# Optimization experiments

Measured on AMD Instinct MI355X. Metric: run time of the kernel, lower is better.

## Reference

```python
import jax, jax.numpy as jnp
import numpy as np

B, LQ, D = 4, 10000, 256
HEADS, LVLS, PTS = 8, 1, 4
HW = 100
LIN = HW * HW


def setup_inputs() -> dict:
    key = jax.random.key(0)
    ks = jax.random.split(key, 14)
    s = 0.02
    ctr = jax.random.uniform(ks[2], (B, LQ, LVLS, 2), jnp.float32)
    wh = 0.05 + 0.2 * jax.random.uniform(ks[3], (B, LQ, LVLS, 2), jnp.float32)
    return {
        "query": jax.random.normal(ks[0], (B, LQ, D), jnp.float32),
        "reference_points": jnp.concatenate([ctr, wh], axis=-1),
        "input_flatten": jax.random.normal(ks[1], (B, LIN, D), jnp.float32),
        "input_spatial_shapes": jnp.array([[HW, HW]], jnp.int32),
        "input_level_start_index": jnp.zeros((LVLS,), jnp.int32),
        "input_padding_mask": jnp.zeros((B, LIN), jnp.bool_),
        "Wv": s * jax.random.normal(ks[4], (D, D), jnp.float32),
        "bv": jnp.zeros((D,), jnp.float32),
        "Woff": s * jax.random.normal(ks[5], (D, HEADS * LVLS * PTS * 2), jnp.float32),
        "boff": s * jax.random.normal(ks[6], (HEADS * LVLS * PTS * 2,), jnp.float32),
        "Wa": s * jax.random.normal(ks[7], (D, HEADS * LVLS * PTS), jnp.float32),
        "ba": jnp.zeros((HEADS * LVLS * PTS,), jnp.float32),
        "Wout": s * jax.random.normal(ks[8], (D, D), jnp.float32),
        "bout": jnp.zeros((D,), jnp.float32),
    }


def _ms_deform_attn(query, reference_points, input_flatten, input_padding_mask,
                    Wv, bv, Woff, boff, Wa, ba, Wout, bout):
    Bn, Lq, Dm = query.shape
    Lin = input_flatten.shape[1]
    Hh, L, P = HEADS, LVLS, PTS
    Cd = Dm // Hh
    # value projection + padding mask
    value = input_flatten @ Wv + bv
    value = jnp.where(input_padding_mask[..., None], 0.0, value)
    # sampling offsets & attention weights
    off = (query @ Woff + boff).reshape(Bn, Lq, Hh, L, P, 2)
    attn = jax.nn.softmax((query @ Wa + ba).reshape(Bn, Lq, Hh, L * P), axis=-1)
    loc = (reference_points[:, :, None, :, None, :2]
           + off / P * reference_points[:, :, None, :, None, 2:] * 0.5)
    # value -> (B*Hh, Cd, Lin); square single-level map H=W=sqrt(Lin)
    v = value.reshape(Bn, Lin, Hh, Cd).transpose(0, 2, 3, 1).reshape(Bn * Hh, Cd, Lin)
    Hs = int(round(Lin ** 0.5)); Ws = Hs
    # level 0 grid: (B*Hh, Lq, P, 2), normalized to [-1, 1]
    g = (2.0 * loc - 1.0)[:, :, :, 0].transpose(0, 2, 1, 3, 4).reshape(Bn * Hh, Lq, P, 2)
    x = (g[..., 0] + 1.0) * Ws / 2.0 - 0.5
    y = (g[..., 1] + 1.0) * Hs / 2.0 - 0.5
    x0 = jnp.floor(x).astype(jnp.int32); y0 = jnp.floor(y).astype(jnp.int32)
    x1 = x0 + 1; y1 = y0 + 1
    wx = x - x0.astype(x.dtype); wy = y - y0.astype(y.dtype)

    def valid(xi, yi):
        return ((xi >= 0) & (xi < Ws) & (yi >= 0) & (yi < Hs)).astype(value.dtype)

    def gather(xi, yi):
        idx = (jnp.clip(yi, 0, Hs - 1) * Ws + jnp.clip(xi, 0, Ws - 1)).reshape(Bn * Hh, 1, Lq * P)
        out = jnp.take_along_axis(v, jnp.broadcast_to(idx, (Bn * Hh, Cd, Lq * P)), axis=2)
        return out.reshape(Bn * Hh, Cd, Lq, P)

    sv = (gather(x0, y0) * ((1 - wx) * (1 - wy) * valid(x0, y0))[:, None]
          + gather(x0, y1) * ((1 - wx) * wy * valid(x0, y1))[:, None]
          + gather(x1, y0) * (wx * (1 - wy) * valid(x1, y0))[:, None]
          + gather(x1, y1) * (wx * wy * valid(x1, y1))[:, None])  # (B*Hh, Cd, Lq, P)
    aw = attn.transpose(0, 2, 1, 3).reshape(Bn * Hh, 1, Lq, L * P)
    out = (sv * aw).sum(-1).reshape(Bn, Hh * Cd, Lq).transpose(0, 2, 1)  # (B, Lq, D)
    return out @ Wout + bout


def reference(query, reference_points, input_flatten, input_spatial_shapes,
              input_level_start_index, input_padding_mask,
              Wv, bv, Woff, boff, Wa, ba, Wout, bout):
    # input_spatial_shapes / level_start_index are redundant here: the core is
    # single-level with H=W=sqrt(Len_in) (faithful to the source code).
    return _ms_deform_attn(query, reference_points, input_flatten, input_padding_mask,
                           Wv, bv, Woff, boff, Wa, ba, Wout, bout)
```

## Files before the change

kernel.cpp:

```cpp
#include <hip/hip_runtime.h>

#define BATCH 4
#define LQ    10000
#define DM    256
#define NH    8
#define NP    4
#define HWD   100
#define LIN   10000

typedef unsigned short ushort_t;
typedef __attribute__((ext_vector_type(8))) short bf16x8;
typedef __attribute__((ext_vector_type(8))) unsigned short u16x8;
typedef __attribute__((ext_vector_type(4))) float f32x4;

__device__ __forceinline__ unsigned short f2bf(float f) {
    unsigned int u = __float_as_uint(f);
    u += 0x7FFFu + ((u >> 16) & 1u);
    return (unsigned short)(u >> 16);
}

__device__ __forceinline__ void gload16(const ushort_t* g, ushort_t* l) {
    __builtin_amdgcn_global_load_lds(
        (const __attribute__((address_space(1))) void*)g,
        (__attribute__((address_space(3))) void*)l, 16, 0, 0);
}

__global__ __launch_bounds__(256) void prep_kernel(
    const float* __restrict__ Wv, const float* __restrict__ Wout,
    const float* __restrict__ Woff, const float* __restrict__ Wa,
    const float* __restrict__ boff, const float* __restrict__ ba,
    ushort_t* __restrict__ WtV, ushort_t* __restrict__ WtO,
    ushort_t* __restrict__ Wcomb, float* __restrict__ bcomb)
{
    const int n = blockIdx.x, k = threadIdx.x;
    const int t32 = k >> 5, lc = (k >> 3) & 3, j = k & 7;
    const int ct = lc ^ ((n >> 1) & 3);
    const size_t addr = (size_t)n * 256 + t32 * 32 + ct * 8 + j;
    if (blockIdx.y == 0) {
        WtV[addr] = f2bf(Wv[(size_t)k * 256 + n]);
    } else if (blockIdx.y == 1) {
        WtO[addr] = f2bf(Wout[(size_t)k * 256 + n]);
    } else if (n < 96) {
        float w = (n < 64) ? Woff[(size_t)k * 64 + n] : Wa[(size_t)k * 32 + (n - 64)];
        Wcomb[addr] = f2bf(w);
        if (k == 0) bcomb[n] = (n < 64) ? boff[n] : ba[n - 64];
    }
}

__global__ __launch_bounds__(256) void gemm_in_kernel(
    const float* __restrict__ flat, const float* __restrict__ query,
    const ushort_t* __restrict__ WtV, const ushort_t* __restrict__ Wcomb,
    const float* __restrict__ bv, const float* __restrict__ bcomb,
    ushort_t* __restrict__ value, float* __restrict__ oaproj)
{
    __shared__ ushort_t As[2][64 * 32];
    __shared__ ushort_t Bs[2][256 * 32];

    const int tid  = threadIdx.x;
    const int lane = tid & 63;
    const int wv   = tid >> 6;

    const int ar  = tid >> 2;
    const int akb = tid & 3;
    const int asw = (akb ^ ((ar >> 1) & 3)) * 8;
    const int fr = lane & 15, kb = lane >> 4;
    const int ln4 = lane >> 2, lc4 = lane & 3;

    if (blockIdx.x < 625) {
        const int row0 = blockIdx.x * 64;
        const float* ap = &flat[(size_t)(row0 + ar) * 256 + akb * 8];
        const f32x4 zero = {0.f, 0.f, 0.f, 0.f};
        f32x4 acc[4][4];
        #pragma unroll
        for (int m = 0; m < 4; ++m)
            #pragma unroll
            for (int n = 0; n < 4; ++n) acc[m][n] = zero;

        {
            float4 f0 = *reinterpret_cast<const float4*>(ap);
            float4 f1 = *reinterpret_cast<const float4*>(ap + 4);
            u16x8 pk;
            pk[0] = f2bf(f0.x); pk[1] = f2bf(f0.y);
            pk[2] = f2bf(f0.z); pk[3] = f2bf(f0.w);
            pk[4] = f2bf(f1.x); pk[5] = f2bf(f1.y);
            pk[6] = f2bf(f1.z); pk[7] = f2bf(f1.w);
            *reinterpret_cast<u16x8*>(&As[0][ar * 32 + asw]) = pk;
            #pragma unroll
            for (int it = 0; it < 4; ++it) {
                int r0 = (it * 4 + wv) * 16;
                gload16(&WtV[(size_t)(r0 + ln4) * 256 + lc4 * 8], &Bs[0][r0 * 32]);
            }
        }
        __syncthreads();

        int c = 0;
        for (int t = 0; t < 8; ++t) {
            const int kn = (t + 1) * 32;
            const bool pf = (t < 7);
            float4 f0, f1;
            if (pf) {
                f0 = *reinterpret_cast<const float4*>(ap + kn);
                f1 = *reinterpret_cast<const float4*>(ap + kn + 4);
                #pragma unroll
                for (int it = 0; it < 4; ++it) {
                    int r0 = (it * 4 + wv) * 16;
                    gload16(&WtV[(size_t)(r0 + ln4) * 256 + kn + lc4 * 8],
                            &Bs[c ^ 1][r0 * 32]);
                }
            }
            bf16x8 af[4], bf[4];
            #pragma unroll
            for (int m = 0; m < 4; ++m) {
                int r = m * 16 + fr;
                af[m] = *reinterpret_cast<const bf16x8*>(
                    &As[c][r * 32 + ((kb ^ ((r >> 1) & 3)) * 8)]);
            }
            #pragma unroll
            for (int n = 0; n < 4; ++n) {
                int cc = wv * 64 + n * 16 + fr;
                bf[n] = *reinterpret_cast<const bf16x8*>(
                    &Bs[c][cc * 32 + ((kb ^ ((cc >> 1) & 3)) * 8)]);
            }
            #pragma unroll
            for (int m = 0; m < 4; ++m)
                #pragma unroll
                for (int n = 0; n < 4; ++n)
                    acc[m][n] = __builtin_amdgcn_mfma_f32_16x16x32_bf16(
                        af[m], bf[n], acc[m][n], 0, 0, 0);
            if (pf) {
                u16x8 pk;
                pk[0] = f2bf(f0.x); pk[1] = f2bf(f0.y);
                pk[2] = f2bf(f0.z); pk[3] = f2bf(f0.w);
                pk[4] = f2bf(f1.x); pk[5] = f2bf(f1.y);
                pk[6] = f2bf(f1.z); pk[7] = f2bf(f1.w);
                *reinterpret_cast<u16x8*>(&As[c ^ 1][ar * 32 + asw]) = pk;
            }
            __syncthreads();
            c ^= 1;
        }

        #pragma unroll
        for (int n = 0; n < 4; ++n) {
            int cc = wv * 64 + n * 16 + fr;
            float bb = bv[cc];
            int hh = cc >> 5, ch = cc & 31;
            #pragma unroll
            for (int m = 0; m < 4; ++m) {
                #pragma unroll
                for (int j = 0; j < 4; ++j) {
                    int r = row0 + m * 16 + kb * 4 + j;
                    int rb = (int)((unsigned)r / 10000u);
                    int pix = r - rb * 10000;
                    size_t addr = (((size_t)(rb * 8 + hh)) * LIN + pix) * 32 + ch;
                    value[addr] = f2bf(acc[m][n][j] + bb);
                }
            }
        }
    } else {
        const int row0 = (blockIdx.x - 625) * 64;
        const float* ap = &query[(size_t)(row0 + ar) * 256 + akb * 8];
        const f32x4 zero = {0.f, 0.f, 0.f, 0.f};
        f32x4 acc[6];
        #pragma unroll
        for (int n = 0; n < 6; ++n) acc[n] = zero;

        {
            float4 f0 = *reinterpret_cast<const float4*>(ap);
            float4 f1 = *reinterpret_cast<const float4*>(ap + 4);
            u16x8 pk;
            pk[0] = f2bf(f0.x); pk[1] = f2bf(f0.y);
            pk[2] = f2bf(f0.z); pk[3] = f2bf(f0.w);
            pk[4] = f2bf(f1.x); pk[5] = f2bf(f1.y);
            pk[6] = f2bf(f1.z); pk[7] = f2bf(f1.w);
            *reinterpret_cast<u16x8*>(&As[0][ar * 32 + asw]) = pk;
            #pragma unroll
            for (int it = 0; it < 2; ++it) {
                int r0 = (it * 4 + wv) * 16;
                if (r0 < 96)
                    gload16(&Wcomb[(size_t)(r0 + ln4) * 256 + lc4 * 8], &Bs[0][r0 * 32]);
            }
        }
        __syncthreads();

        int c = 0;
        for (int t = 0; t < 8; ++t) {
            const int kn = (t + 1) * 32;
            const bool pf = (t < 7);
            float4 f0, f1;
            if (pf) {
                f0 = *reinterpret_cast<const float4*>(ap + kn);
                f1 = *reinterpret_cast<const float4*>(ap + kn + 4);
                #pragma unroll
                for (int it = 0; it < 2; ++it) {
                    int r0 = (it * 4 + wv) * 16;
                    if (r0 < 96)
                        gload16(&Wcomb[(size_t)(r0 + ln4) * 256 + kn + lc4 * 8],
                                &Bs[c ^ 1][r0 * 32]);
                }
            }
            bf16x8 af;
            {
                int r = wv * 16 + fr;
                af = *reinterpret_cast<const bf16x8*>(
                    &As[c][r * 32 + ((kb ^ ((r >> 1) & 3)) * 8)]);
            }
            #pragma unroll
            for (int n = 0; n < 6; ++n) {
                int cc = n * 16 + fr;
                bf16x8 bf = *reinterpret_cast<const bf16x8*>(
                    &Bs[c][cc * 32 + ((kb ^ ((cc >> 1) & 3)) * 8)]);
                acc[n] = __builtin_amdgcn_mfma_f32_16x16x32_bf16(
                    af, bf, acc[n], 0, 0, 0);
            }
            if (pf) {
                u16x8 pk;
                pk[0] = f2bf(f0.x); pk[1] = f2bf(f0.y);
                pk[2] = f2bf(f0.z); pk[3] = f2bf(f0.w);
                pk[4] = f2bf(f1.x); pk[5] = f2bf(f1.y);
                pk[6] = f2bf(f1.z); pk[7] = f2bf(f1.w);
                *reinterpret_cast<u16x8*>(&As[c ^ 1][ar * 32 + asw]) = pk;
            }
            __syncthreads();
            c ^= 1;
        }

        #pragma unroll
        for (int n = 0; n < 6; ++n) {
            int cc = n * 16 + fr;
            float bb = bcomb[cc];
            #pragma unroll
            for (int j = 0; j < 4; ++j) {
                int r = row0 + wv * 16 + kb * 4 + j;
                oaproj[(size_t)r * 96 + cc] = acc[n][j] + bb;
            }
        }
    }
}

__global__ __launch_bounds__(256, 4) void deform_kernel(
    const float* __restrict__ oaproj, const float* __restrict__ refpts,
    const ushort_t* __restrict__ value, ushort_t* __restrict__ out)
{
    __shared__ int4   soff[NP * 64];
    __shared__ float4 swt [NP * 64];

    const int blk = blockIdx.x;
    const int xcd = blk & 7;
    const int sub = (blk >> 3) & 3;
    const int chunk = blk >> 5;
    const int map = xcd * 4 + sub;
    const int b = map >> 3, h = map & 7;
    const int q0 = chunk * 64;

    const int tid = threadIdx.x;

    if (tid < 64) {
        const int qg = q0 + tid;
        if (qg >= LQ) {
            int4 zi = {0, 0, 0, 0};
            float4 zf = {0.f, 0.f, 0.f, 0.f};
            #pragma unroll
            for (int p = 0; p < NP; ++p) { soff[p * 64 + tid] = zi; swt[p * 64 + tid] = zf; }
        } else {
            const size_t row = (size_t)b * LQ + qg;
            const float* oa = oaproj + row * 96;
            float4 l4 = *reinterpret_cast<const float4*>(oa + 64 + h * 4);
            float mx = fmaxf(fmaxf(l4.x, l4.y), fmaxf(l4.z, l4.w));
            float e0 = __expf(l4.x - mx), e1 = __expf(l4.y - mx);
            float e2 = __expf(l4.z - mx), e3 = __expf(l4.w - mx);
            float inv = 1.f / (e0 + e1 + e2 + e3);
            float ew[4] = {e0 * inv, e1 * inv, e2 * inv, e3 * inv};
            float4 o0 = *reinterpret_cast<const float4*>(oa + h * 8);
            float4 o1 = *reinterpret_cast<const float4*>(oa + h * 8 + 4);
            float oxv[4] = {o0.x, o0.z, o1.x, o1.z};
            float oyv[4] = {o0.y, o0.w, o1.y, o1.w};
            const float* rp = refpts + row * 4;
            float cx = rp[0], cy = rp[1], rw = rp[2], rh = rp[3];
            #pragma unroll
            for (int p = 0; p < NP; ++p) {
                float x = (cx + oxv[p] * rw * 0.125f) * (float)HWD - 0.5f;
                float y = (cy + oyv[p] * rh * 0.125f) * (float)HWD - 0.5f;
                float x0f = floorf(x), y0f = floorf(y);
                float wx = x - x0f, wy = y - y0f;
                int x0 = (int)x0f, y0 = (int)y0f;
                int x1 = x0 + 1, y1 = y0 + 1;
                float vx0 = (x0 >= 0 && x0 < HWD) ? 1.f : 0.f;
                float vx1 = (x1 >= 0 && x1 < HWD) ? 1.f : 0.f;
                float vy0 = (y0 >= 0 && y0 < HWD) ? 1.f : 0.f;
                float vy1 = (y1 >= 0 && y1 < HWD) ? 1.f : 0.f;
                int cx0 = min(max(x0, 0), HWD - 1), cx1 = min(max(x1, 0), HWD - 1);
                int cy0 = min(max(y0, 0), HWD - 1), cy1 = min(max(y1, 0), HWD - 1);
                float aw = ew[p];
                int4 of = {cy0 * HWD + cx0, cy0 * HWD + cx1,
                           cy1 * HWD + cx0, cy1 * HWD + cx1};
                float4 wt = {aw * (1.f - wx) * (1.f - wy) * vx0 * vy0,
                             aw * wx * (1.f - wy) * vx1 * vy0,
                             aw * (1.f - wx) * wy * vx0 * vy1,
                             aw * wx * wy * vx1 * vy1};
                soff[p * 64 + tid] = of;
                swt [p * 64 + tid] = wt;
            }
        }
    }
    __syncthreads();

    const int q = tid >> 2, c8 = tid & 3;
    const int qg = q0 + q;
    const ushort_t* vb = value + (size_t)map * (LIN * 32) + c8 * 8;

    int4 of[4]; float4 w4[4];
    #pragma unroll
    for (int p = 0; p < NP; ++p) {
        of[p] = soff[p * 64 + q];
        w4[p] = swt [p * 64 + q];
    }
    uint4 vv[4][4];
    #pragma unroll
    for (int p = 0; p < NP; ++p) {
        vv[p][0] = *reinterpret_cast<const uint4*>(vb + ((size_t)of[p].x << 5));
        vv[p][1] = *reinterpret_cast<const uint4*>(vb + ((size_t)of[p].y << 5));
        vv[p][2] = *reinterpret_cast<const uint4*>(vb + ((size_t)of[p].z << 5));
        vv[p][3] = *reinterpret_cast<const uint4*>(vb + ((size_t)of[p].w << 5));
    }
    float a0 = 0.f, a1 = 0.f, a2 = 0.f, a3 = 0.f;
    float a4 = 0.f, a5 = 0.f, a6 = 0.f, a7 = 0.f;
    #define ACC(V, W) { const float w_ = (W); const uint4 v_ = (V); \
        a0 += w_ * __uint_as_float(v_.x << 16); \
        a1 += w_ * __uint_as_float(v_.x & 0xffff0000u); \
        a2 += w_ * __uint_as_float(v_.y << 16); \
        a3 += w_ * __uint_as_float(v_.y & 0xffff0000u); \
        a4 += w_ * __uint_as_float(v_.z << 16); \
        a5 += w_ * __uint_as_float(v_.z & 0xffff0000u); \
        a6 += w_ * __uint_as_float(v_.w << 16); \
        a7 += w_ * __uint_as_float(v_.w & 0xffff0000u); }
    #pragma unroll
    for (int p = 0; p < NP; ++p) {
        ACC(vv[p][0], w4[p].x);
        ACC(vv[p][1], w4[p].y);
        ACC(vv[p][2], w4[p].z);
        ACC(vv[p][3], w4[p].w);
    }
    #undef ACC

    if (qg < LQ) {
        const size_t orow = (size_t)b * LQ + qg;
        u16x8 pk;
        pk[0] = f2bf(a0); pk[1] = f2bf(a1);
        pk[2] = f2bf(a2); pk[3] = f2bf(a3);
        pk[4] = f2bf(a4); pk[5] = f2bf(a5);
        pk[6] = f2bf(a6); pk[7] = f2bf(a7);
        const int cc = h * 4 + c8;
        const int t32 = cc >> 2;
        const int ct = (cc & 3) ^ ((int)(orow >> 1) & 3);
        *reinterpret_cast<u16x8*>(&out[orow * 256 + t32 * 32 + ct * 8]) = pk;
    }
}

__global__ __launch_bounds__(256) void gemm_out_kernel(
    const ushort_t* __restrict__ A, const ushort_t* __restrict__ Wt,
    const float* __restrict__ bias, float* __restrict__ Cout)
{
    __shared__ ushort_t As[2][64 * 32];
    __shared__ ushort_t Bs[2][256 * 32];

    const int tid  = threadIdx.x;
    const int lane = tid & 63;
    const int wv   = tid >> 6;
    const int row0 = blockIdx.x * 64;

    const f32x4 zero = {0.f, 0.f, 0.f, 0.f};
    f32x4 acc[4][4];
    #pragma unroll
    for (int m = 0; m < 4; ++m)
        #pragma unroll
        for (int n = 0; n < 4; ++n) acc[m][n] = zero;

    const int fr = lane & 15, kb = lane >> 4;
    const int ln4 = lane >> 2, lc4 = lane & 3;

    {
        gload16(&A[(size_t)(row0 + wv * 16 + ln4) * 256 + lc4 * 8],
                &As[0][wv * 512]);
        #pragma unroll
        for (int it = 0; it < 4; ++it) {
            int r0 = (it * 4 + wv) * 16;
            gload16(&Wt[(size_t)(r0 + ln4) * 256 + lc4 * 8], &Bs[0][r0 * 32]);
        }
    }
    __syncthreads();

    int c = 0;
    for (int t = 0; t < 8; ++t) {
        const int kn = (t + 1) * 32;
        if (t < 7) {
            gload16(&A[(size_t)(row0 + wv * 16 + ln4) * 256 + kn + lc4 * 8],
                    &As[c ^ 1][wv * 512]);
            #pragma unroll
            for (int it = 0; it < 4; ++it) {
                int r0 = (it * 4 + wv) * 16;
                gload16(&Wt[(size_t)(r0 + ln4) * 256 + kn + lc4 * 8],
                        &Bs[c ^ 1][r0 * 32]);
            }
        }
        bf16x8 af[4], bf[4];
        #pragma unroll
        for (int m = 0; m < 4; ++m) {
            int r = m * 16 + fr;
            af[m] = *reinterpret_cast<const bf16x8*>(
                &As[c][r * 32 + ((kb ^ ((r >> 1) & 3)) * 8)]);
        }
        #pragma unroll
        for (int n = 0; n < 4; ++n) {
            int cc = wv * 64 + n * 16 + fr;
            bf[n] = *reinterpret_cast<const bf16x8*>(
                &Bs[c][cc * 32 + ((kb ^ ((cc >> 1) & 3)) * 8)]);
        }
        #pragma unroll
        for (int m = 0; m < 4; ++m)
            #pragma unroll
            for (int n = 0; n < 4; ++n)
                acc[m][n] = __builtin_amdgcn_mfma_f32_16x16x32_bf16(
                    af[m], bf[n], acc[m][n], 0, 0, 0);
        __syncthreads();
        c ^= 1;
    }

    #pragma unroll
    for (int m = 0; m < 4; ++m) {
        #pragma unroll
        for (int n = 0; n < 4; ++n) {
            int cc = wv * 64 + n * 16 + fr;
            float bb = bias[cc];
            #pragma unroll
            for (int j = 0; j < 4; ++j) {
                int r = row0 + m * 16 + kb * 4 + j;
                Cout[(size_t)r * 256 + cc] = acc[m][n][j] + bb;
            }
        }
    }
}

extern "C" void kernel_launch(void* const* d_in, const int* in_sizes, int n_in,
                              void* d_out, int out_size, void* d_ws, size_t ws_size,
                              hipStream_t stream)
{
    const float* query  = (const float*)d_in[0];
    const float* refpts = (const float*)d_in[1];
    const float* flat   = (const float*)d_in[2];
    const float* Wv   = (const float*)d_in[6];
    const float* bv   = (const float*)d_in[7];
    const float* Woff = (const float*)d_in[8];
    const float* boff = (const float*)d_in[9];
    const float* Wa   = (const float*)d_in[10];
    const float* ba   = (const float*)d_in[11];
    const float* Wout = (const float*)d_in[12];
    const float* bout = (const float*)d_in[13];
    float* out = (float*)d_out;

    const size_t MROWS = (size_t)BATCH * LIN;
    ushort_t* value  = (ushort_t*)d_ws;
    ushort_t* ws2    = value + MROWS * DM;
    ushort_t* WtV    = ws2 + MROWS * DM;
    ushort_t* WtO    = WtV + 256 * 256;
    ushort_t* Wcomb  = WtO + 256 * 256;
    float*    bcomb  = (float*)(Wcomb + 96 * 256);
    float*    oaproj = bcomb + 128;

    dim3 blk(256);

    prep_kernel<<<dim3(256, 3), blk, 0, stream>>>(
        Wv, Wout, Woff, Wa, boff, ba, WtV, WtO, Wcomb, bcomb);

    gemm_in_kernel<<<dim3(1250), blk, 0, stream>>>(
        flat, query, WtV, Wcomb, bv, bcomb, value, oaproj);

    deform_kernel<<<dim3(157 * 32), blk, 0, stream>>>(
        oaproj, refpts, value, ws2);

    gemm_out_kernel<<<dim3(MROWS / 64), blk, 0, stream>>>(
        ws2, WtO, bout, out);
}
```

Baseline: 70.91 us.

## Deepen A-operand prefetch to two stages with explicit vmcnt waits in projection GEMM

The projection GEMM now loads fp32 activation tiles two K-steps ahead into registers and converts them to bf16 into LDS one step ahead. __syncthreads is replaced by explicit s_waitcnt vmcnt/lgkmcnt plus a raw barrier, so the next A tile's global loads can stay in flight across the barrier. The K loop is fully unrolled. The aim is to hide global-load latency behind MFMA work. In exchange it adds register pressure and depends on correct manual vmcnt accounting: a wrong count would race with the global_load_lds writes.

Result: no change. 71.99 us (+1.5%).

```diff
diff --git a/kernel.cpp b/kernel.cpp
--- a/kernel.cpp
+++ b/kernel.cpp
@@ -19,11 +19,25 @@
     return (unsigned short)(u >> 16);
 }
 
+__device__ __forceinline__ u16x8 pack8(float4 f0, float4 f1) {
+    u16x8 pk;
+    pk[0] = f2bf(f0.x); pk[1] = f2bf(f0.y);
+    pk[2] = f2bf(f0.z); pk[3] = f2bf(f0.w);
+    pk[4] = f2bf(f1.x); pk[5] = f2bf(f1.y);
+    pk[6] = f2bf(f1.z); pk[7] = f2bf(f1.w);
+    return pk;
+}
+
 __device__ __forceinline__ void gload16(const ushort_t* g, ushort_t* l) {
     __builtin_amdgcn_global_load_lds(
         (const __attribute__((address_space(1))) void*)g,
         (__attribute__((address_space(3))) void*)l, 16, 0, 0);
 }
+
+#define WAIT_VM2()  asm volatile("s_waitcnt vmcnt(2)" ::: "memory")
+#define WAIT_VM0()  asm volatile("s_waitcnt vmcnt(0)" ::: "memory")
+#define WAIT_LGKM() asm volatile("s_waitcnt lgkmcnt(0)" ::: "memory")
+#define BARRIER()   { __builtin_amdgcn_s_barrier(); __builtin_amdgcn_sched_barrier(0); }
 
 __global__ __launch_bounds__(256) void prep_kernel(
     const float* __restrict__ Wv, const float* __restrict__ Wout,
@@ -76,38 +90,41 @@
             #pragma unroll
             for (int n = 0; n < 4; ++n) acc[m][n] = zero;
 
+        float4 an0[2], an1[2];
+
         {
             float4 f0 = *reinterpret_cast<const float4*>(ap);
             float4 f1 = *reinterpret_cast<const float4*>(ap + 4);
-            u16x8 pk;
-            pk[0] = f2bf(f0.x); pk[1] = f2bf(f0.y);
-            pk[2] = f2bf(f0.z); pk[3] = f2bf(f0.w);
-            pk[4] = f2bf(f1.x); pk[5] = f2bf(f1.y);
-            pk[6] = f2bf(f1.z); pk[7] = f2bf(f1.w);
-            *reinterpret_cast<u16x8*>(&As[0][ar * 32 + asw]) = pk;
             #pragma unroll
             for (int it = 0; it < 4; ++it) {
                 int r0 = (it * 4 + wv) * 16;
                 gload16(&WtV[(size_t)(r0 + ln4) * 256 + lc4 * 8], &Bs[0][r0 * 32]);
             }
-        }
-        __syncthreads();
-
-        int c = 0;
+            *reinterpret_cast<u16x8*>(&As[0][ar * 32 + asw]) = pack8(f0, f1);
+            an0[1] = *reinterpret_cast<const float4*>(ap + 32);
+            an1[1] = *reinterpret_cast<const float4*>(ap + 36);
+        }
+        WAIT_VM2(); WAIT_LGKM(); BARRIER();
+
+        #pragma unroll
         for (int t = 0; t < 8; ++t) {
-            const int kn = (t + 1) * 32;
-            const bool pf = (t < 7);
-            float4 f0, f1;
-            if (pf) {
-                f0 = *reinterpret_cast<const float4*>(ap + kn);
-                f1 = *reinterpret_cast<const float4*>(ap + kn + 4);
+            const int c = t & 1;
+            if (t + 1 < 8) {
                 #pragma unroll
                 for (int it = 0; it < 4; ++it) {
                     int r0 = (it * 4 + wv) * 16;
-                    gload16(&WtV[(size_t)(r0 + ln4) * 256 + kn + lc4 * 8],
+                    gload16(&WtV[(size_t)(r0 + ln4) * 256 + (t + 1) * 32 + lc4 * 8],
                             &Bs[c ^ 1][r0 * 32]);
                 }
             }
+            if (t + 2 < 8) {
+                an0[c] = *reinterpret_cast<const float4*>(ap + (t + 2) * 32);
+                an1[c] = *reinterpret_cast<const float4*>(ap + (t + 2) * 32 + 4);
+            }
+            if (t + 1 < 8)
+                *reinterpret_cast<u16x8*>(&As[c ^ 1][ar * 32 + asw]) =
+                    pack8(an0[c ^ 1], an1[c ^ 1]);
+
             bf16x8 af[4], bf[4];
             #pragma unroll
             for (int m = 0; m < 4; ++m) {
@@ -127,16 +144,9 @@
                 for (int n = 0; n < 4; ++n)
                     acc[m][n] = __builtin_amdgcn_mfma_f32_16x16x32_bf16(
                         af[m], bf[n], acc[m][n], 0, 0, 0);
-            if (pf) {
-                u16x8 pk;
-                pk[0] = f2bf(f0.x); pk[1] = f2bf(f0.y);
-                pk[2] = f2bf(f0.z); pk[3] = f2bf(f0.w);
-                pk[4] = f2bf(f1.x); pk[5] = f2bf(f1.y);
-                pk[6] = f2bf(f1.z); pk[7] = f2bf(f1.w);
-                *reinterpret_cast<u16x8*>(&As[c ^ 1][ar * 32 + asw]) = pk;
-            }
-            __syncthreads();
-            c ^= 1;
+
+            if (t < 6) { WAIT_VM2(); } else { WAIT_VM0(); }
+            WAIT_LGKM(); BARRIER();
         }
 
         #pragma unroll
@@ -164,40 +174,43 @@
         #pragma unroll
         for (int n = 0; n < 6; ++n) acc[n] = zero;
 
+        float4 an0[2], an1[2];
+
         {
             float4 f0 = *reinterpret_cast<const float4*>(ap);
             float4 f1 = *reinterpret_cast<const float4*>(ap + 4);
-            u16x8 pk;
-            pk[0] = f2bf(f0.x); pk[1] = f2bf(f0.y);
-            pk[2] = f2bf(f0.z); pk[3] = f2bf(f0.w);
-            pk[4] = f2bf(f1.x); pk[5] = f2bf(f1.y);
-            pk[6] = f2bf(f1.z); pk[7] = f2bf(f1.w);
-            *reinterpret_cast<u16x8*>(&As[0][ar * 32 + asw]) = pk;
             #pragma unroll
             for (int it = 0; it < 2; ++it) {
                 int r0 = (it * 4 + wv) * 16;
                 if (r0 < 96)
                     gload16(&Wcomb[(size_t)(r0 + ln4) * 256 + lc4 * 8], &Bs[0][r0 * 32]);
             }
-        }
-        __syncthreads();
-
-        int c = 0;
+            *reinterpret_cast<u16x8*>(&As[0][ar * 32 + asw]) = pack8(f0, f1);
+            an0[1] = *reinterpret_cast<const float4*>(ap + 32);
+            an1[1] = *reinterpret_cast<const float4*>(ap + 36);
+        }
+        WAIT_VM2(); WAIT_LGKM(); BARRIER();
+
+        #pragma unroll
         for (int t = 0; t < 8; ++t) {
-            const int kn = (t + 1) * 32;
-            const bool pf = (t < 7);
-            float4 f0, f1;
-            if (pf) {
-                f0 = *reinterpret_cast<const float4*>(ap + kn);
-                f1 = *reinterpret_cast<const float4*>(ap + kn + 4);
+            const int c = t & 1;
+            if (t + 1 < 8) {
                 #pragma unroll
                 for (int it = 0; it < 2; ++it) {
                     int r0 = (it * 4 + wv) * 16;
                     if (r0 < 96)
-                        gload16(&Wcomb[(size_t)(r0 + ln4) * 256 + kn + lc4 * 8],
+                        gload16(&Wcomb[(size_t)(r0 + ln4) * 256 + (t + 1) * 32 + lc4 * 8],
                                 &Bs[c ^ 1][r0 * 32]);
                 }
             }
+            if (t + 2 < 8) {
+                an0[c] = *reinterpret_cast<const float4*>(ap + (t + 2) * 32);
+                an1[c] = *reinterpret_cast<const float4*>(ap + (t + 2) * 32 + 4);
+            }
+            if (t + 1 < 8)
+                *reinterpret_cast<u16x8*>(&As[c ^ 1][ar * 32 + asw]) =
+                    pack8(an0[c ^ 1], an1[c ^ 1]);
+
             bf16x8 af;
             {
                 int r = wv * 16 + fr;
@@ -212,16 +225,9 @@
                 acc[n] = __builtin_amdgcn_mfma_f32_16x16x32_bf16(
                     af, bf, acc[n], 0, 0, 0);
             }
-            if (pf) {
-                u16x8 pk;
-                pk[0] = f2bf(f0.x); pk[1] = f2bf(f0.y);
-                pk[2] = f2bf(f0.z); pk[3] = f2bf(f0.w);
-                pk[4] = f2bf(f1.x); pk[5] = f2bf(f1.y);
-                pk[6] = f2bf(f1.z); pk[7] = f2bf(f1.w);
-                *reinterpret_cast<u16x8*>(&As[c ^ 1][ar * 32 + asw]) = pk;
-            }
-            __syncthreads();
-            c ^= 1;
+
+            if (t < 6) { WAIT_VM2(); } else { WAIT_VM0(); }
+            WAIT_LGKM(); BARRIER();
         }
 
         #pragma unroll
```

## Split GEMM tiles to 64x128 columns and unify value/query projection paths

Applied to the files above, without the earlier changes.

Both the input projection and output projection GEMMs now use 64x128 output tiles instead of 64x256, doubling the block count. The value and query projections share one code path, and the query projection now spreads its 96 output columns across all four waves instead of splitting rows by wave. This is meant to raise occupancy and parallelism through smaller LDS and accumulator footprints, and to balance the query blocks. In exchange, A tiles (including the fp32-to-bf16 conversion of flat) are loaded and converted twice per row block.

Measured after the change: 78.76 us. 11.1% more time.

```diff
diff --git a/kernel.cpp b/kernel.cpp
--- a/kernel.cpp
+++ b/kernel.cpp
@@ -17,6 +17,15 @@
     unsigned int u = __float_as_uint(f);
     u += 0x7FFFu + ((u >> 16) & 1u);
     return (unsigned short)(u >> 16);
+}
+
+__device__ __forceinline__ u16x8 pack8(float4 f0, float4 f1) {
+    u16x8 pk;
+    pk[0] = f2bf(f0.x); pk[1] = f2bf(f0.y);
+    pk[2] = f2bf(f0.z); pk[3] = f2bf(f0.w);
+    pk[4] = f2bf(f1.x); pk[5] = f2bf(f1.y);
+    pk[6] = f2bf(f1.z); pk[7] = f2bf(f1.w);
+    return pk;
 }
 
 __device__ __forceinline__ void gload16(const ushort_t* g, ushort_t* l) {
@@ -54,7 +63,7 @@
     ushort_t* __restrict__ value, float* __restrict__ oaproj)
 {
     __shared__ ushort_t As[2][64 * 32];
-    __shared__ ushort_t Bs[2][256 * 32];
+    __shared__ ushort_t Bs[2][128 * 32];
 
     const int tid  = threadIdx.x;
     const int lane = tid & 63;
@@ -66,82 +75,80 @@
     const int fr = lane & 15, kb = lane >> 4;
     const int ln4 = lane >> 2, lc4 = lane & 3;
 
-    if (blockIdx.x < 625) {
-        const int row0 = blockIdx.x * 64;
-        const float* ap = &flat[(size_t)(row0 + ar) * 256 + akb * 8];
-        const f32x4 zero = {0.f, 0.f, 0.f, 0.f};
-        f32x4 acc[4][4];
+    const bool isVal = (blockIdx.x < 1250);
+    const int row0 = isVal ? (blockIdx.x >> 1) * 64 : (blockIdx.x - 1250) * 64;
+    const int col0 = isVal ? (blockIdx.x & 1) * 128 : 0;
+    const float* ap = isVal ? &flat [(size_t)(row0 + ar) * 256 + akb * 8]
+                            : &query[(size_t)(row0 + ar) * 256 + akb * 8];
+    const ushort_t* Wt = isVal ? WtV : Wcomb;
+    const int nrows = isVal ? 128 : 96;
+
+    const f32x4 zero = {0.f, 0.f, 0.f, 0.f};
+    f32x4 acc[4][2];
+    #pragma unroll
+    for (int m = 0; m < 4; ++m)
+        #pragma unroll
+        for (int n = 0; n < 2; ++n) acc[m][n] = zero;
+
+    {
+        float4 f0 = *reinterpret_cast<const float4*>(ap);
+        float4 f1 = *reinterpret_cast<const float4*>(ap + 4);
+        #pragma unroll
+        for (int it = 0; it < 2; ++it) {
+            int r0 = (it * 4 + wv) * 16;
+            if (r0 < nrows)
+                gload16(&Wt[(size_t)(col0 + r0 + ln4) * 256 + lc4 * 8],
+                        &Bs[0][r0 * 32]);
+        }
+        *reinterpret_cast<u16x8*>(&As[0][ar * 32 + asw]) = pack8(f0, f1);
+    }
+    __syncthreads();
+
+    int c = 0;
+    for (int t = 0; t < 8; ++t) {
+        const int kn = (t + 1) * 32;
+        const bool pf = (t < 7);
+        float4 f0, f1;
+        if (pf) {
+            f0 = *reinterpret_cast<const float4*>(ap + kn);
+            f1 = *reinterpret_cast<const float4*>(ap + kn + 4);
+            #pragma unroll
+            for (int it = 0; it < 2; ++it) {
+                int r0 = (it * 4 + wv) * 16;
+                if (r0 < nrows)
+                    gload16(&Wt[(size_t)(col0 + r0 + ln4) * 256 + kn + lc4 * 8],
+                            &Bs[c ^ 1][r0 * 32]);
+            }
+        }
+        bf16x8 af[4], bf[2];
+        #pragma unroll
+        for (int m = 0; m < 4; ++m) {
+            int r = m * 16 + fr;
+            af[m] = *reinterpret_cast<const bf16x8*>(
+                &As[c][r * 32 + ((kb ^ ((r >> 1) & 3)) * 8)]);
+        }
+        #pragma unroll
+        for (int n = 0; n < 2; ++n) {
+            int lr = wv * 32 + n * 16 + fr;
+            bf[n] = *reinterpret_cast<const bf16x8*>(
+                &Bs[c][lr * 32 + ((kb ^ ((lr >> 1) & 3)) * 8)]);
+        }
         #pragma unroll
         for (int m = 0; m < 4; ++m)
             #pragma unroll
-            for (int n = 0; n < 4; ++n) acc[m][n] = zero;
-
-        {
-            float4 f0 = *reinterpret_cast<const float4*>(ap);
-            float4 f1 = *reinterpret_cast<const float4*>(ap + 4);
-            u16x8 pk;
-            pk[0] = f2bf(f0.x); pk[1] = f2bf(f0.y);
-            pk[2] = f2bf(f0.z); pk[3] = f2bf(f0.w);
-            pk[4] = f2bf(f1.x); pk[5] = f2bf(f1.y);
-            pk[6] = f2bf(f1.z); pk[7] = f2bf(f1.w);
-            *reinterpret_cast<u16x8*>(&As[0][ar * 32 + asw]) = pk;
-            #pragma unroll
-            for (int it = 0; it < 4; ++it) {
-                int r0 = (it * 4 + wv) * 16;
-                gload16(&WtV[(size_t)(r0 + ln4) * 256 + lc4 * 8], &Bs[0][r0 * 32]);
-            }
-        }
+            for (int n = 0; n < 2; ++n)
+                acc[m][n] = __builtin_amdgcn_mfma_f32_16x16x32_bf16(
+                    af[m], bf[n], acc[m][n], 0, 0, 0);
+        if (pf)
+            *reinterpret_cast<u16x8*>(&As[c ^ 1][ar * 32 + asw]) = pack8(f0, f1);
         __syncthreads();
-
-        int c = 0;
-        for (int t = 0; t < 8; ++t) {
-            const int kn = (t + 1) * 32;
-            const bool pf = (t < 7);
-            float4 f0, f1;
-            if (pf) {
-                f0 = *reinterpret_cast<const float4*>(ap + kn);
-                f1 = *reinterpret_cast<const float4*>(ap + kn + 4);
-                #pragma unroll
-                for (int it = 0; it < 4; ++it) {
-                    int r0 = (it * 4 + wv) * 16;
-                    gload16(&WtV[(size_t)(r0 + ln4) * 256 + kn + lc4 * 8],
-                            &Bs[c ^ 1][r0 * 32]);
-                }
-            }
-            bf16x8 af[4], bf[4];
-            #pragma unroll
-            for (int m = 0; m < 4; ++m) {
-                int r = m * 16 + fr;
-                af[m] = *reinterpret_cast<const bf16x8*>(
-                    &As[c][r * 32 + ((kb ^ ((r >> 1) & 3)) * 8)]);
-            }
-            #pragma unroll
-            for (int n = 0; n < 4; ++n) {
-                int cc = wv * 64 + n * 16 + fr;
-                bf[n] = *reinterpret_cast<const bf16x8*>(
-                    &Bs[c][cc * 32 + ((kb ^ ((cc >> 1) & 3)) * 8)]);
-            }
-            #pragma unroll
-            for (int m = 0; m < 4; ++m)
-                #pragma unroll
-                for (int n = 0; n < 4; ++n)
-                    acc[m][n] = __builtin_amdgcn_mfma_f32_16x16x32_bf16(
-                        af[m], bf[n], acc[m][n], 0, 0, 0);
-            if (pf) {
-                u16x8 pk;
-                pk[0] = f2bf(f0.x); pk[1] = f2bf(f0.y);
-                pk[2] = f2bf(f0.z); pk[3] = f2bf(f0.w);
-                pk[4] = f2bf(f1.x); pk[5] = f2bf(f1.y);
-                pk[6] = f2bf(f1.z); pk[7] = f2bf(f1.w);
-                *reinterpret_cast<u16x8*>(&As[c ^ 1][ar * 32 + asw]) = pk;
-            }
-            __syncthreads();
-            c ^= 1;
-        }
-
-        #pragma unroll
-        for (int n = 0; n < 4; ++n) {
-            int cc = wv * 64 + n * 16 + fr;
+        c ^= 1;
+    }
+
+    if (isVal) {
+        #pragma unroll
+        for (int n = 0; n < 2; ++n) {
+            int cc = col0 + wv * 32 + n * 16 + fr;
             float bb = bv[cc];
             int hh = cc >> 5, ch = cc & 31;
             #pragma unroll
@@ -157,81 +164,19 @@
             }
         }
     } else {
-        const int row0 = (blockIdx.x - 625) * 64;
-        const float* ap = &query[(size_t)(row0 + ar) * 256 + akb * 8];
-        const f32x4 zero = {0.f, 0.f, 0.f, 0.f};
-        f32x4 acc[6];
-        #pragma unroll
-        for (int n = 0; n < 6; ++n) acc[n] = zero;
-
-        {
-            float4 f0 = *reinterpret_cast<const float4*>(ap);
-            float4 f1 = *reinterpret_cast<const float4*>(ap + 4);
-            u16x8 pk;
-            pk[0] = f2bf(f0.x); pk[1] = f2bf(f0.y);
-            pk[2] = f2bf(f0.z); pk[3] = f2bf(f0.w);
-            pk[4] = f2bf(f1.x); pk[5] = f2bf(f1.y);
-            pk[6] = f2bf(f1.z); pk[7] = f2bf(f1.w);
-            *reinterpret_cast<u16x8*>(&As[0][ar * 32 + asw]) = pk;
-            #pragma unroll
-            for (int it = 0; it < 2; ++it) {
-                int r0 = (it * 4 + wv) * 16;
-                if (r0 < 96)
-                    gload16(&Wcomb[(size_t)(r0 + ln4) * 256 + lc4 * 8], &Bs[0][r0 * 32]);
-            }
-        }
-        __syncthreads();
-
-        int c = 0;
-        for (int t = 0; t < 8; ++t) {
-            const int kn = (t + 1) * 32;
-            const bool pf = (t < 7);
-            float4 f0, f1;
-            if (pf) {
-                f0 = *reinterpret_cast<const float4*>(ap + kn);
-                f1 = *reinterpret_cast<const float4*>(ap + kn + 4);
+        #pragma unroll
+        for (int n = 0; n < 2; ++n) {
+            int cc = wv * 32 + n * 16 + fr;
+            if (cc < 96) {
+                float bb = bcomb[cc];
                 #pragma unroll
-                for (int it = 0; it < 2; ++it) {
-                    int r0 = (it * 4 + wv) * 16;
-                    if (r0 < 96)
-                        gload16(&Wcomb[(size_t)(r0 + ln4) * 256 + kn + lc4 * 8],
-                                &Bs[c ^ 1][r0 * 32]);
+                for (int m = 0; m < 4; ++m) {
+                    #pragma unroll
+                    for (int j = 0; j < 4; ++j) {
+                        int r = row0 + m * 16 + kb * 4 + j;
+                        oaproj[(size_t)r * 96 + cc] = acc[m][n][j] + bb;
+                    }
                 }
-            }
-            bf16x8 af;
-            {
-                int r = wv * 16 + fr;
-                af = *reinterpret_cast<const bf16x8*>(
-                    &As[c][r * 32 + ((kb ^ ((r >> 1) & 3)) * 8)]);
-            }
-            #pragma unroll
-            for (int n = 0; n < 6; ++n) {
-                int cc = n * 16 + fr;
-                bf16x8 bf = *reinterpret_cast<const bf16x8*>(
-                    &Bs[c][cc * 32 + ((kb ^ ((cc >> 1) & 3)) * 8)]);
-                acc[n] = __builtin_amdgcn_mfma_f32_16x16x32_bf16(
-                    af, bf, acc[n], 0, 0, 0);
-            }
-            if (pf) {
-                u16x8 pk;
-                pk[0] = f2bf(f0.x); pk[1] = f2bf(f0.y);
-                pk[2] = f2bf(f0.z); pk[3] = f2bf(f0.w);
-                pk[4] = f2bf(f1.x); pk[5] = f2bf(f1.y);
-                pk[6] = f2bf(f1.z); pk[7] = f2bf(f1.w);
-                *reinterpret_cast<u16x8*>(&As[c ^ 1][ar * 32 + asw]) = pk;
-            }
-            __syncthreads();
-            c ^= 1;
-        }
-
-        #pragma unroll
-        for (int n = 0; n < 6; ++n) {
-            int cc = n * 16 + fr;
-            float bb = bcomb[cc];
-            #pragma unroll
-            for (int j = 0; j < 4; ++j) {
-                int r = row0 + wv * 16 + kb * 4 + j;
-                oaproj[(size_t)r * 96 + cc] = acc[n][j] + bb;
             }
         }
     }
@@ -361,19 +306,20 @@
     const float* __restrict__ bias, float* __restrict__ Cout)
 {
     __shared__ ushort_t As[2][64 * 32];
-    __shared__ ushort_t Bs[2][256 * 32];
+    __shared__ ushort_t Bs[2][128 * 32];
 
     const int tid  = threadIdx.x;
     const int lane = tid & 63;
     const int wv   = tid >> 6;
-    const int row0 = blockIdx.x * 64;
+    const int row0 = (blockIdx.x >> 1) * 64;
+    const int col0 = (blockIdx.x & 1) * 128;
 
     const f32x4 zero = {0.f, 0.f, 0.f, 0.f};
-    f32x4 acc[4][4];
+    f32x4 acc[4][2];
     #pragma unroll
     for (int m = 0; m < 4; ++m)
         #pragma unroll
-        for (int n = 0; n < 4; ++n) acc[m][n] = zero;
+        for (int n = 0; n < 2; ++n) acc[m][n] = zero;
 
     const int fr = lane & 15, kb = lane >> 4;
     const int ln4 = lane >> 2, lc4 = lane & 3;
@@ -382,9 +328,9 @@
         gload16(&A[(size_t)(row0 + wv * 16 + ln4) * 256 + lc4 * 8],
                 &As[0][wv * 512]);
         #pragma unroll
-        for (int it = 0; it < 4; ++it) {
+        for (int it = 0; it < 2; ++it) {
             int r0 = (it * 4 + wv) * 16;
-            gload16(&Wt[(size_t)(r0 + ln4) * 256 + lc4 * 8], &Bs[0][r0 * 32]);
+            gload16(&Wt[(size_t)(col0 + r0 + ln4) * 256 + lc4 * 8], &Bs[0][r0 * 32]);
         }
     }
     __syncthreads();
@@ -396,13 +342,13 @@
             gload16(&A[(size_t)(row0 + wv * 16 + ln4) * 256 + kn + lc4 * 8],
                     &As[c ^ 1][wv * 512]);
             #pragma unroll
-            for (int it = 0; it < 4; ++it) {
+            for (int it = 0; it < 2; ++it) {
                 int r0 = (it * 4 + wv) * 16;
-                gload16(&Wt[(size_t)(r0 + ln4) * 256 + kn + lc4 * 8],
+                gload16(&Wt[(size_t)(col0 + r0 + ln4) * 256 + kn + lc4 * 8],
                         &Bs[c ^ 1][r0 * 32]);
             }
         }
-        bf16x8 af[4], bf[4];
+        bf16x8 af[4], bf[2];
         #pragma unroll
         for (int m = 0; m < 4; ++m) {
             int r = m * 16 + fr;
@@ -410,15 +356,15 @@
                 &As[c][r * 32 + ((kb ^ ((r >> 1) & 3)) * 8)]);
         }
         #pragma unroll
-        for (int n = 0; n < 4; ++n) {
-            int cc = wv * 64 + n * 16 + fr;
+        for (int n = 0; n < 2; ++n) {
+            int lr = wv * 32 + n * 16 + fr;
             bf[n] = *reinterpret_cast<const bf16x8*>(
-                &Bs[c][cc * 32 + ((kb ^ ((cc >> 1) & 3)) * 8)]);
+                &Bs[c][lr * 32 + ((kb ^ ((lr >> 1) & 3)) * 8)]);
         }
         #pragma unroll
         for (int m = 0; m < 4; ++m)
             #pragma unroll
-            for (int n = 0; n < 4; ++n)
+            for (int n = 0; n < 2; ++n)
                 acc[m][n] = __builtin_amdgcn_mfma_f32_16x16x32_bf16(
                     af[m], bf[n], acc[m][n], 0, 0, 0);
         __syncthreads();
@@ -428,8 +374,8 @@
     #pragma unroll
     for (int m = 0; m < 4; ++m) {
         #pragma unroll
-        for (int n = 0; n < 4; ++n) {
-            int cc = wv * 64 + n * 16 + fr;
+        for (int n = 0; n < 2; ++n) {
+            int cc = col0 + wv * 32 + n * 16 + fr;
             float bb = bias[cc];
             #pragma unroll
             for (int j = 0; j < 4; ++j) {
@@ -471,12 +417,12 @@
     prep_kernel<<<dim3(256, 3), blk, 0, stream>>>(
         Wv, Wout, Woff, Wa, boff, ba, WtV, WtO, Wcomb, bcomb);
 
-    gemm_in_kernel<<<dim3(1250), blk, 0, stream>>>(
+    gemm_in_kernel<<<dim3(1875), blk, 0, stream>>>(
         flat, query, WtV, Wcomb, bv, bcomb, value, oaproj);
 
     deform_kernel<<<dim3(157 * 32), blk, 0, stream>>>(
         oaproj, refpts, value, ws2);
 
-    gemm_out_kernel<<<dim3(MROWS / 64), blk, 0, stream>>>(
+    gemm_out_kernel<<<dim3(1250), blk, 0, stream>>>(
         ws2, WtO, bout, out);
 }
```
